# Optimization experiments

Measured on AMD Instinct MI355X. Metric: run time of the kernel, lower is better.

The kernel has to match this reference:

```python
import jax, jax.numpy as jnp
import numpy as np

N = 16384  # number of internal DAG nodes
L = 16384  # number of leaves


def setup_inputs() -> dict:
    key = jax.random.key(0)
    ks = jax.random.split(key, 12)
    idx = jnp.arange(N)
    # internal-child offsets and leaf ids
    off_l = jax.random.randint(ks[0], (N,), 1, N)
    off_r = jax.random.randint(ks[1], (N,), 1, N)
    leaf_l = jax.random.randint(ks[2], (N,), 0, L)
    leaf_r = jax.random.randint(ks[3], (N,), 0, L)
    is_int_l = (jax.random.uniform(ks[4], (N,)) < 0.5) & (idx < N - 1)
    is_int_r = (jax.random.uniform(ks[5], (N,)) < 0.5) & (idx < N - 1)
    # forward-pointing DAG: internal child index strictly greater than parent
    left = jnp.where(is_int_l, jnp.clip(idx + off_l, 0, N - 1), -(leaf_l + 1)).astype(jnp.int32)
    right = jnp.where(is_int_r, jnp.clip(idx + off_r, 0, N - 1), -(leaf_r + 1)).astype(jnp.int32)
    return {
        "thresholds": jax.random.normal(ks[6], (N,), dtype=jnp.float32),
        "rules": jax.random.randint(ks[7], (N,), 0, 16).astype(jnp.int32),
        "binary_ops": jax.random.randint(ks[8], (N,), 0, 8).astype(jnp.int32),
        "left": left,
        "right": right,
        "leaf_is_reroll": jax.random.uniform(ks[9], (L,)) < 0.5,
        "leaf_mask_left": jax.random.randint(ks[10], (L,), 0, 64).astype(jnp.int32),
        "leaf_mask_right": jax.random.randint(ks[11], (L,), 0, 64).astype(jnp.int32),
        "leaf_mask_op": jax.random.randint(jax.random.fold_in(key, 100), (L,), 0, 4).astype(jnp.int32),
        "leaf_score_cat": jax.random.randint(jax.random.fold_in(key, 101), (L,), 0, 16).astype(jnp.int32),
    }


def _active_mask(left, right, n_nodes):
    def step(reachable, _):
        active_left = jnp.where(reachable & (left >= 0), left, n_nodes)
        active_right = jnp.where(reachable & (right >= 0), right, n_nodes)
        new_reachable = jnp.zeros(n_nodes + 1, dtype=jnp.bool_)
        new_reachable = new_reachable.at[active_left].set(True)
        new_reachable = new_reachable.at[active_right].set(True)
        new_reachable = new_reachable.at[0].set(True)
        return new_reachable[:n_nodes] | reachable, None

    init = jnp.zeros(n_nodes, dtype=jnp.bool_).at[0].set(True)
    mask, _ = jax.lax.scan(step, init, None, length=n_nodes)
    return mask


def _subtree_leaf_flags(left, right, leaf_is_reroll, n):
    def is_leaf_score(child):
        leaf_id = -child - 1
        return (child < 0) & (~leaf_is_reroll[leaf_id])

    def is_leaf_reroll(child):
        leaf_id = -child - 1
        return (child < 0) & leaf_is_reroll[leaf_id]

    def step(carry, i):
        has_score, has_reroll = carry
        node = n - 1 - i  # postorder: children have larger indices
        l, r = left[node], right[node]

        def child_has_score(child):
            return is_leaf_score(child) | jnp.where(child >= 0, has_score[child], False)

        def child_has_reroll(child):
            return is_leaf_reroll(child) | jnp.where(child >= 0, has_reroll[child], False)

        has_score = has_score.at[node].set(child_has_score(l) | child_has_score(r))
        has_reroll = has_reroll.at[node].set(child_has_reroll(l) | child_has_reroll(r))
        return (has_score, has_reroll), None

    init = (jnp.zeros(n, dtype=jnp.bool_), jnp.zeros(n, dtype=jnp.bool_))
    (has_score, has_reroll), _ = jax.lax.scan(step, init, jnp.arange(n))
    return has_score, has_reroll


def reference(thresholds, rules, binary_ops, left, right, leaf_is_reroll,
              leaf_mask_left, leaf_mask_right, leaf_mask_op, leaf_score_cat):
    n = rules.shape[0]
    active_mask = _active_mask(left, right, n)
    has_score, has_reroll = _subtree_leaf_flags(left, right, leaf_is_reroll, n)
    active_node_count = jnp.sum(active_mask)
    return active_mask, has_score, has_reroll, active_node_count
```

## Files before the change

kernel.cpp:

```cpp
#include <hip/hip_runtime.h>

#define NN 16384
#define NT 1024
#define PER 16

__global__ __launch_bounds__(NT) void dag_eval_kernel(
    const int* __restrict__ left,
    const int* __restrict__ right,
    const unsigned char* __restrict__ reroll_raw,
    int* __restrict__ out)
{
    __shared__ __align__(16) unsigned char reach[NN];
    __shared__ __align__(16) unsigned char state[NN + 16];
    __shared__ int flags[4];
    __shared__ int nzmask;
    __shared__ int cnt;

    const int tid = threadIdx.x;
    const int b0  = tid * PER;

    if (tid < 4)  flags[tid] = 0;
    if (tid == 0) { nzmask = 0; cnt = 0; }
    if (tid < 16) state[NN + tid] = 4;

    unsigned int cpair[PER];
    {
        const int4* l4 = (const int4*)left;
        const int4* r4 = (const int4*)right;
        #pragma unroll
        for (int j = 0; j < PER / 4; ++j) {
            int4 a = l4[(b0 >> 2) + j];
            int4 b = r4[(b0 >> 2) + j];
            cpair[4*j+0] = (a.x & 0xFFFFu) | ((unsigned)b.x << 16);
            cpair[4*j+1] = (a.y & 0xFFFFu) | ((unsigned)b.y << 16);
            cpair[4*j+2] = (a.z & 0xFFFFu) | ((unsigned)b.z << 16);
            cpair[4*j+3] = (a.w & 0xFFFFu) | ((unsigned)b.w << 16);
        }
    }

    {
        uint4 v = ((const uint4*)reroll_raw)[tid];
        unsigned int t = v.x | v.y | v.z | v.w;
        unsigned int m = 0;
        if (t & 0x000000FFu) m |= 1u;
        if (t & 0x0000FF00u) m |= 2u;
        if (t & 0x00FF0000u) m |= 4u;
        if (t & 0xFF000000u) m |= 8u;
        if (m) atomicOr(&nzmask, (int)m);
    }
    *(uint4*)&reach[b0] = make_uint4(0u, 0u, 0u, 0u);
    __syncthreads();

    const int mask   = nzmask;
    const int layout = ((mask & ~1) == 0) ? 0 : (((mask & 3) == 0) ? 1 : 2);
    const int*   ri = (const int*)reroll_raw;
    const float* rf = (const float*)reroll_raw;

    int sreg[PER];
    unsigned int todo = 0;
    #pragma unroll
    for (int k = 0; k < PER; ++k) {
        int c0 = (int)(short)(cpair[k] & 0xFFFFu);
        int c1 = (int)(short)(cpair[k] >> 16);
        int s = 0;
        if (c0 < 0) {
            int id = -c0 - 1;
            bool rr = (layout == 2) ? (reroll_raw[id] != 0)
                     : (layout == 1) ? (rf[id] != 0.0f)
                                     : (ri[id] != 0);
            s |= rr ? 2 : 1;
        }
        if (c1 < 0) {
            int id = -c1 - 1;
            bool rr = (layout == 2) ? (reroll_raw[id] != 0)
                     : (layout == 1) ? (rf[id] != 0.0f)
                                     : (ri[id] != 0);
            s |= rr ? 2 : 1;
        }
        if ((c0 < 0 && c1 < 0) || s == 3) s |= 4;
        else todo |= 1u << k;
        sreg[k] = s;
        state[b0 + k] = (unsigned char)s;
    }
    if (tid == 0) reach[0] = 1;
    __syncthreads();

    unsigned int pushed = 0, mm = 0;
    for (int w = 0; w < 4096; ++w) {
        bool ch = false;

        uint4 rv = *(const uint4*)&reach[b0];
        mm  =  ((rv.x * 0x01020408u) >> 24) & 0xFu;
        mm |= (((rv.y * 0x01020408u) >> 24) & 0xFu) << 4;
        mm |= (((rv.z * 0x01020408u) >> 24) & 0xFu) << 8;
        mm |= (((rv.w * 0x01020408u) >> 24) & 0xFu) << 12;
        unsigned int newp = mm & ~pushed;
        if (newp) {
            pushed |= newp;
            ch = true;
            #pragma unroll
            for (int k = 0; k < PER; ++k) {
                if ((newp >> k) & 1u) {
                    int c0 = (int)(short)(cpair[k] & 0xFFFFu);
                    int c1 = (int)(short)(cpair[k] >> 16);
                    if (c0 > 0) reach[c0] = (unsigned char)1;
                    if (c1 > 0) reach[c1] = (unsigned char)1;
                }
            }
        }

        if (todo) {
            int tl[PER], tr[PER];
            #pragma unroll
            for (int k = 0; k < PER; ++k) {
                bool act = (todo >> k) & 1u;
                int c0 = (int)(short)(cpair[k] & 0xFFFFu);
                int c1 = (int)(short)(cpair[k] >> 16);
                int la = (act && c0 > 0) ? c0 : NN;
                int ra = (act && c1 > 0) ? c1 : NN;
                tl[k] = state[la];
                tr[k] = state[ra];
            }
            #pragma unroll
            for (int k = 0; k < PER; ++k) {
                if ((todo >> k) & 1u) {
                    int sl = tl[k], sr = tr[k];
                    int ns = sreg[k] | (sl & 3) | (sr & 3);
                    bool fin = ((sl & sr & 4) != 0) || ((ns & 3) == 3);
                    if (fin) { ns |= 4; todo &= ~(1u << k); }
                    if (ns != sreg[k]) {
                        sreg[k] = ns;
                        state[b0 + k] = (unsigned char)ns;
                        ch = true;
                    }
                }
            }
        }

        if (ch) flags[w & 3] = 1;
        __syncthreads();
        int f = flags[w & 3];
        if (tid == 0) flags[(w + 2) & 3] = 0;
        if (!f) break;
    }

    int cc = __popc(mm);
    #pragma unroll
    for (int off = 32; off; off >>= 1) cc += __shfl_down(cc, off);
    if ((tid & 63) == 0) atomicAdd(&cnt, cc);

    int4* out4 = (int4*)out;
    #pragma unroll
    for (int j = 0; j < PER / 4; ++j) {
        int4 a, h, r;
        a.x = (mm >> (4*j+0)) & 1; a.y = (mm >> (4*j+1)) & 1;
        a.z = (mm >> (4*j+2)) & 1; a.w = (mm >> (4*j+3)) & 1;
        h.x =  sreg[4*j+0] & 1;       h.y =  sreg[4*j+1] & 1;
        h.z =  sreg[4*j+2] & 1;       h.w =  sreg[4*j+3] & 1;
        r.x = (sreg[4*j+0] >> 1) & 1; r.y = (sreg[4*j+1] >> 1) & 1;
        r.z = (sreg[4*j+2] >> 1) & 1; r.w = (sreg[4*j+3] >> 1) & 1;
        out4[(b0 >> 2) + j]            = a;
        out4[((NN + b0) >> 2) + j]     = h;
        out4[((2 * NN + b0) >> 2) + j] = r;
    }
    __syncthreads();
    if (tid == 0) out[3 * NN] = cnt;
}

extern "C" void kernel_launch(void* const* d_in, const int* in_sizes, int n_in,
                              void* d_out, int out_size, void* d_ws, size_t ws_size,
                              hipStream_t stream)
{
    const int* left  = (const int*)d_in[3];
    const int* right = (const int*)d_in[4];
    const unsigned char* reroll = (const unsigned char*)d_in[5];
    int* out = (int*)d_out;
    dag_eval_kernel<<<1, NT, 0, stream>>>(left, right, reroll, out);
}
```

Before: 32.84 us.

## Switch to strided node-to-thread mapping and restructure the fixpoint sweep

Nodes are now assigned to threads as tid + k*NT instead of contiguous blocks of 16. This makes the global loads of left/right coalesced and spreads shared-memory byte accesses across banks. The sweep now reads reach per node, in pairs, and updates state from high k to low k so that changes can propagate within one sweep. Final outputs and the count are rebuilt from the shared reach and state arrays, and the iteration cap is lowered to 600. The trade-off is more per-byte LDS reads than the old single uint4 load, and a cap that depends on the DAG depth staying small.

```diff
diff --git a/kernel.cpp b/kernel.cpp
--- a/kernel.cpp
+++ b/kernel.cpp
@@ -2,7 +2,6 @@
 
 #define NN 16384
 #define NT 1024
-#define PER 16
 
 __global__ __launch_bounds__(NT) void dag_eval_kernel(
     const int* __restrict__ left,
@@ -17,25 +16,17 @@
     __shared__ int cnt;
 
     const int tid = threadIdx.x;
-    const int b0  = tid * PER;
 
     if (tid < 4)  flags[tid] = 0;
     if (tid == 0) { nzmask = 0; cnt = 0; }
     if (tid < 16) state[NN + tid] = 4;
 
-    unsigned int cpair[PER];
-    {
-        const int4* l4 = (const int4*)left;
-        const int4* r4 = (const int4*)right;
-        #pragma unroll
-        for (int j = 0; j < PER / 4; ++j) {
-            int4 a = l4[(b0 >> 2) + j];
-            int4 b = r4[(b0 >> 2) + j];
-            cpair[4*j+0] = (a.x & 0xFFFFu) | ((unsigned)b.x << 16);
-            cpair[4*j+1] = (a.y & 0xFFFFu) | ((unsigned)b.y << 16);
-            cpair[4*j+2] = (a.z & 0xFFFFu) | ((unsigned)b.z << 16);
-            cpair[4*j+3] = (a.w & 0xFFFFu) | ((unsigned)b.w << 16);
-        }
+    unsigned int cpair[16];
+    #pragma unroll
+    for (int k = 0; k < 16; ++k) {
+        int l = left[tid + k * NT];
+        int r = right[tid + k * NT];
+        cpair[k] = (l & 0xFFFFu) | ((unsigned)r << 16);
     }
 
     {
@@ -48,7 +39,7 @@
         if (t & 0xFF000000u) m |= 8u;
         if (m) atomicOr(&nzmask, (int)m);
     }
-    *(uint4*)&reach[b0] = make_uint4(0u, 0u, 0u, 0u);
+    *(uint4*)&reach[tid * 16] = make_uint4(0u, 0u, 0u, 0u);
     __syncthreads();
 
     const int mask   = nzmask;
@@ -56,10 +47,10 @@
     const int*   ri = (const int*)reroll_raw;
     const float* rf = (const float*)reroll_raw;
 
-    int sreg[PER];
+    int sreg[16];
     unsigned int todo = 0;
     #pragma unroll
-    for (int k = 0; k < PER; ++k) {
+    for (int k = 0; k < 16; ++k) {
         int c0 = (int)(short)(cpair[k] & 0xFFFFu);
         int c1 = (int)(short)(cpair[k] >> 16);
         int s = 0;
@@ -80,29 +71,33 @@
         if ((c0 < 0 && c1 < 0) || s == 3) s |= 4;
         else todo |= 1u << k;
         sreg[k] = s;
-        state[b0 + k] = (unsigned char)s;
+        state[tid + k * NT] = (unsigned char)s;
     }
     if (tid == 0) reach[0] = 1;
     __syncthreads();
 
-    unsigned int pushed = 0, mm = 0;
-    for (int w = 0; w < 4096; ++w) {
+    unsigned int pushed = 0;
+    for (int w = 0; w < 600; ++w) {
         bool ch = false;
 
-        uint4 rv = *(const uint4*)&reach[b0];
-        mm  =  ((rv.x * 0x01020408u) >> 24) & 0xFu;
-        mm |= (((rv.y * 0x01020408u) >> 24) & 0xFu) << 4;
-        mm |= (((rv.z * 0x01020408u) >> 24) & 0xFu) << 8;
-        mm |= (((rv.w * 0x01020408u) >> 24) & 0xFu) << 12;
-        unsigned int newp = mm & ~pushed;
-        if (newp) {
-            pushed |= newp;
-            ch = true;
-            #pragma unroll
-            for (int k = 0; k < PER; ++k) {
-                if ((newp >> k) & 1u) {
-                    int c0 = (int)(short)(cpair[k] & 0xFFFFu);
-                    int c1 = (int)(short)(cpair[k] >> 16);
+        #pragma unroll
+        for (int kp = 0; kp < 8; ++kp) {
+            const int k0 = 2 * kp, k1 = 2 * kp + 1;
+            unsigned int need = (~pushed >> k0) & 3u;
+            if (need) {
+                int r0 = (need & 1u) ? (int)reach[tid + k0 * NT] : 0;
+                int r1 = (need & 2u) ? (int)reach[tid + k1 * NT] : 0;
+                if (r0) {
+                    pushed |= 1u << k0; ch = true;
+                    int c0 = (int)(short)(cpair[k0] & 0xFFFFu);
+                    int c1 = (int)(short)(cpair[k0] >> 16);
+                    if (c0 > 0) reach[c0] = (unsigned char)1;
+                    if (c1 > 0) reach[c1] = (unsigned char)1;
+                }
+                if (r1) {
+                    pushed |= 1u << k1; ch = true;
+                    int c0 = (int)(short)(cpair[k1] & 0xFFFFu);
+                    int c1 = (int)(short)(cpair[k1] >> 16);
                     if (c0 > 0) reach[c0] = (unsigned char)1;
                     if (c1 > 0) reach[c1] = (unsigned char)1;
                 }
@@ -110,28 +105,39 @@
         }
 
         if (todo) {
-            int tl[PER], tr[PER];
             #pragma unroll
-            for (int k = 0; k < PER; ++k) {
-                bool act = (todo >> k) & 1u;
-                int c0 = (int)(short)(cpair[k] & 0xFFFFu);
-                int c1 = (int)(short)(cpair[k] >> 16);
-                int la = (act && c0 > 0) ? c0 : NN;
-                int ra = (act && c1 > 0) ? c1 : NN;
-                tl[k] = state[la];
-                tr[k] = state[ra];
-            }
-            #pragma unroll
-            for (int k = 0; k < PER; ++k) {
-                if ((todo >> k) & 1u) {
-                    int sl = tl[k], sr = tr[k];
-                    int ns = sreg[k] | (sl & 3) | (sr & 3);
-                    bool fin = ((sl & sr & 4) != 0) || ((ns & 3) == 3);
-                    if (fin) { ns |= 4; todo &= ~(1u << k); }
-                    if (ns != sreg[k]) {
-                        sreg[k] = ns;
-                        state[b0 + k] = (unsigned char)ns;
-                        ch = true;
+            for (int kp = 7; kp >= 0; --kp) {
+                const int k0 = 2 * kp, k1 = 2 * kp + 1;
+                if ((todo >> k0) & 3u) {
+                    bool a1 = (todo >> k1) & 1u;
+                    bool a0 = (todo >> k0) & 1u;
+                    int c10 = (int)(short)(cpair[k1] & 0xFFFFu);
+                    int c11 = (int)(short)(cpair[k1] >> 16);
+                    int c00 = (int)(short)(cpair[k0] & 0xFFFFu);
+                    int c01 = (int)(short)(cpair[k0] >> 16);
+                    int sl1 = state[(a1 && c10 > 0) ? c10 : NN];
+                    int sr1 = state[(a1 && c11 > 0) ? c11 : NN];
+                    int sl0 = state[(a0 && c00 > 0) ? c00 : NN];
+                    int sr0 = state[(a0 && c01 > 0) ? c01 : NN];
+                    if (a1) {
+                        int ns = sreg[k1] | (sl1 & 3) | (sr1 & 3);
+                        bool fin = ((sl1 & sr1 & 4) != 0) || ((ns & 3) == 3);
+                        if (fin) { ns |= 4; todo &= ~(1u << k1); }
+                        if (ns != sreg[k1]) {
+                            sreg[k1] = ns;
+                            state[tid + k1 * NT] = (unsigned char)ns;
+                            ch = true;
+                        }
+                    }
+                    if (a0) {
+                        int ns = sreg[k0] | (sl0 & 3) | (sr0 & 3);
+                        bool fin = ((sl0 & sr0 & 4) != 0) || ((ns & 3) == 3);
+                        if (fin) { ns |= 4; todo &= ~(1u << k0); }
+                        if (ns != sreg[k0]) {
+                            sreg[k0] = ns;
+                            state[tid + k0 * NT] = (unsigned char)ns;
+                            ch = true;
+                        }
                     }
                 }
             }
@@ -144,24 +150,41 @@
         if (!f) break;
     }
 
-    int cc = __popc(mm);
-    #pragma unroll
-    for (int off = 32; off; off >>= 1) cc += __shfl_down(cc, off);
-    if ((tid & 63) == 0) atomicAdd(&cnt, cc);
+    uint4 v = *(const uint4*)&reach[tid * 16];
+    {
+        unsigned int t = v.x + v.y + v.z + v.w;
+        int cc = (t & 0xFF) + ((t >> 8) & 0xFF) + ((t >> 16) & 0xFF) + (t >> 24);
+        #pragma unroll
+        for (int off = 32; off; off >>= 1) cc += __shfl_down(cc, off);
+        if ((tid & 63) == 0) atomicAdd(&cnt, cc);
+    }
 
     int4* out4 = (int4*)out;
-    #pragma unroll
-    for (int j = 0; j < PER / 4; ++j) {
-        int4 a, h, r;
-        a.x = (mm >> (4*j+0)) & 1; a.y = (mm >> (4*j+1)) & 1;
-        a.z = (mm >> (4*j+2)) & 1; a.w = (mm >> (4*j+3)) & 1;
-        h.x =  sreg[4*j+0] & 1;       h.y =  sreg[4*j+1] & 1;
-        h.z =  sreg[4*j+2] & 1;       h.w =  sreg[4*j+3] & 1;
-        r.x = (sreg[4*j+0] >> 1) & 1; r.y = (sreg[4*j+1] >> 1) & 1;
-        r.z = (sreg[4*j+2] >> 1) & 1; r.w = (sreg[4*j+3] >> 1) & 1;
-        out4[(b0 >> 2) + j]            = a;
-        out4[((NN + b0) >> 2) + j]     = h;
-        out4[((2 * NN + b0) >> 2) + j] = r;
+    {
+        unsigned int wd[4] = {v.x, v.y, v.z, v.w};
+        #pragma unroll
+        for (int j = 0; j < 4; ++j) {
+            int4 a;
+            a.x = (wd[j] >> 0)  & 1;
+            a.y = (wd[j] >> 8)  & 1;
+            a.z = (wd[j] >> 16) & 1;
+            a.w = (wd[j] >> 24) & 1;
+            out4[(tid * 16 >> 2) + j] = a;
+        }
+    }
+    {
+        uint4 sv = *(const uint4*)&state[tid * 16];
+        unsigned int wd[4] = {sv.x, sv.y, sv.z, sv.w};
+        #pragma unroll
+        for (int j = 0; j < 4; ++j) {
+            int4 h, r;
+            h.x = (wd[j] >> 0)  & 1; h.y = (wd[j] >> 8)  & 1;
+            h.z = (wd[j] >> 16) & 1; h.w = (wd[j] >> 24) & 1;
+            r.x = (wd[j] >> 1)  & 1; r.y = (wd[j] >> 9)  & 1;
+            r.z = (wd[j] >> 17) & 1; r.w = (wd[j] >> 25) & 1;
+            out4[((NN + tid * 16) >> 2) + j]     = h;
+            out4[((2 * NN + tid * 16) >> 2) + j] = r;
+        }
     }
     __syncthreads();
     if (tid == 0) out[3 * NN] = cnt;
```

New measurement: 36.30 us. 10.6% more time.

## Propagate reachability and subtree flags two levels per iteration via shared child pairs

Applied to the files above, without the earlier changes.

Stores the packed child pairs for every node in shared memory so each sweep can look at grandchildren. Reachability propagation marks children and grandchildren, and the subtree-flag fixpoint reads grandchild states, which roughly halves the number of barrier-synchronised iterations needed to converge. Per-child pending bits let a node finish once each child is done, and the change flag now fires only on real updates. The cost is 64KB more shared memory, extra shared loads per iteration, and an iteration cap lowered to 600, which could cut off deep DAGs before they converge.

```diff
diff --git a/kernel.cpp b/kernel.cpp
--- a/kernel.cpp
+++ b/kernel.cpp
@@ -10,6 +10,7 @@
     const unsigned char* __restrict__ reroll_raw,
     int* __restrict__ out)
 {
+    __shared__ __align__(16) unsigned int  pairs[NN];
     __shared__ __align__(16) unsigned char reach[NN];
     __shared__ __align__(16) unsigned char state[NN + 16];
     __shared__ int flags[4];
@@ -21,7 +22,7 @@
 
     if (tid < 4)  flags[tid] = 0;
     if (tid == 0) { nzmask = 0; cnt = 0; }
-    if (tid < 16) state[NN + tid] = 4;
+    if (tid < 16) state[NN + tid] = 0;
 
     unsigned int cpair[PER];
     {
@@ -35,6 +36,8 @@
             cpair[4*j+1] = (a.y & 0xFFFFu) | ((unsigned)b.y << 16);
             cpair[4*j+2] = (a.z & 0xFFFFu) | ((unsigned)b.z << 16);
             cpair[4*j+3] = (a.w & 0xFFFFu) | ((unsigned)b.w << 16);
+            *(uint4*)&pairs[b0 + 4*j] = make_uint4(cpair[4*j+0], cpair[4*j+1],
+                                                   cpair[4*j+2], cpair[4*j+3]);
         }
     }
 
@@ -57,28 +60,29 @@
     const float* rf = (const float*)reroll_raw;
 
     int sreg[PER];
-    unsigned int todo = 0;
+    unsigned int todo = 0, pend = 0;
     #pragma unroll
     for (int k = 0; k < PER; ++k) {
         int c0 = (int)(short)(cpair[k] & 0xFFFFu);
         int c1 = (int)(short)(cpair[k] >> 16);
         int s = 0;
+        unsigned int p2 = 0;
         if (c0 < 0) {
             int id = -c0 - 1;
             bool rr = (layout == 2) ? (reroll_raw[id] != 0)
                      : (layout == 1) ? (rf[id] != 0.0f)
                                      : (ri[id] != 0);
             s |= rr ? 2 : 1;
-        }
+        } else p2 |= 1u;
         if (c1 < 0) {
             int id = -c1 - 1;
             bool rr = (layout == 2) ? (reroll_raw[id] != 0)
                      : (layout == 1) ? (rf[id] != 0.0f)
                                      : (ri[id] != 0);
             s |= rr ? 2 : 1;
-        }
-        if ((c0 < 0 && c1 < 0) || s == 3) s |= 4;
-        else todo |= 1u << k;
+        } else p2 |= 2u;
+        if (p2 == 0u || s == 3) s |= 4;
+        else { todo |= 1u << k; pend |= p2 << (2 * k); }
         sreg[k] = s;
         state[b0 + k] = (unsigned char)s;
     }
@@ -86,7 +90,7 @@
     __syncthreads();
 
     unsigned int pushed = 0, mm = 0;
-    for (int w = 0; w < 4096; ++w) {
+    for (int w = 0; w < 600; ++w) {
         bool ch = false;
 
         uint4 rv = *(const uint4*)&reach[b0];
@@ -97,37 +101,65 @@
         unsigned int newp = mm & ~pushed;
         if (newp) {
             pushed |= newp;
-            ch = true;
             #pragma unroll
             for (int k = 0; k < PER; ++k) {
                 if ((newp >> k) & 1u) {
                     int c0 = (int)(short)(cpair[k] & 0xFFFFu);
                     int c1 = (int)(short)(cpair[k] >> 16);
-                    if (c0 > 0) reach[c0] = (unsigned char)1;
-                    if (c1 > 0) reach[c1] = (unsigned char)1;
+                    if (c0 > 0) {
+                        if (reach[c0] == 0) { reach[c0] = 1; ch = true; }
+                        unsigned int pr = pairs[c0];
+                        int g0 = (int)(short)(pr & 0xFFFFu);
+                        int g1 = (int)(short)(pr >> 16);
+                        if (g0 > 0 && reach[g0] == 0) { reach[g0] = 1; ch = true; }
+                        if (g1 > 0 && reach[g1] == 0) { reach[g1] = 1; ch = true; }
+                    }
+                    if (c1 > 0) {
+                        if (reach[c1] == 0) { reach[c1] = 1; ch = true; }
+                        unsigned int pr = pairs[c1];
+                        int g0 = (int)(short)(pr & 0xFFFFu);
+                        int g1 = (int)(short)(pr >> 16);
+                        if (g0 > 0 && reach[g0] == 0) { reach[g0] = 1; ch = true; }
+                        if (g1 > 0 && reach[g1] == 0) { reach[g1] = 1; ch = true; }
+                    }
                 }
             }
         }
 
         if (todo) {
-            int tl[PER], tr[PER];
-            #pragma unroll
-            for (int k = 0; k < PER; ++k) {
-                bool act = (todo >> k) & 1u;
-                int c0 = (int)(short)(cpair[k] & 0xFFFFu);
-                int c1 = (int)(short)(cpair[k] >> 16);
-                int la = (act && c0 > 0) ? c0 : NN;
-                int ra = (act && c1 > 0) ? c1 : NN;
-                tl[k] = state[la];
-                tr[k] = state[ra];
-            }
             #pragma unroll
             for (int k = 0; k < PER; ++k) {
                 if ((todo >> k) & 1u) {
-                    int sl = tl[k], sr = tr[k];
+                    unsigned int p2 = (pend >> (2 * k)) & 3u;
+                    int c0 = (int)(short)(cpair[k] & 0xFFFFu);
+                    int c1 = (int)(short)(cpair[k] >> 16);
+                    int sl = state[(p2 & 1u) ? c0 : NN];
+                    int sr = state[(p2 & 2u) ? c1 : NN];
                     int ns = sreg[k] | (sl & 3) | (sr & 3);
-                    bool fin = ((sl & sr & 4) != 0) || ((ns & 3) == 3);
+                    unsigned int np2 = p2;
+                    if ((p2 & 1u) && (sl & 4)) np2 &= ~1u;
+                    if ((p2 & 2u) && (sr & 4)) np2 &= ~2u;
+                    if (np2 & 1u) {
+                        unsigned int pr = pairs[c0];
+                        int g0 = (int)(short)(pr & 0xFFFFu);
+                        int g1 = (int)(short)(pr >> 16);
+                        int s0 = (g0 > 0) ? (int)state[g0] : 4;
+                        int s1 = (g1 > 0) ? (int)state[g1] : 4;
+                        ns |= (s0 & 3) | (s1 & 3);
+                        if (s0 & s1 & 4) np2 &= ~1u;
+                    }
+                    if (np2 & 2u) {
+                        unsigned int pr = pairs[c1];
+                        int g0 = (int)(short)(pr & 0xFFFFu);
+                        int g1 = (int)(short)(pr >> 16);
+                        int s0 = (g0 > 0) ? (int)state[g0] : 4;
+                        int s1 = (g1 > 0) ? (int)state[g1] : 4;
+                        ns |= (s0 & 3) | (s1 & 3);
+                        if (s0 & s1 & 4) np2 &= ~2u;
+                    }
+                    bool fin = (np2 == 0u) || ((ns & 3) == 3);
                     if (fin) { ns |= 4; todo &= ~(1u << k); }
+                    pend = (pend & ~(3u << (2 * k))) | (np2 << (2 * k));
                     if (ns != sreg[k]) {
                         sreg[k] = ns;
                         state[b0 + k] = (unsigned char)ns;
```

Result: no change. 32.91 us (+0.2%).

## Switch to single-wavefront sparse frontier/worklist phase after fixed block sweeps

Applied to the files above, without the earlier changes.

Runs a fixed number of block-wide sweeps, then gathers unfinished nodes into a shared worklist. A single 64-lane wavefront finishes both the reachability propagation, using a shared bitmask with atomicOr, and the subtree-flag fixpoint without block barriers. The aim is to remove the many block-wide __syncthreads iterations of the long convergence tail. The cost is serial work on one wavefront and a hard 300-iteration cap, which could leave the result unconverged on deep chains; it also relies on intra-wave visibility of shared memory.

```diff
diff --git a/kernel.cpp b/kernel.cpp
--- a/kernel.cpp
+++ b/kernel.cpp
@@ -3,6 +3,7 @@
 #define NN 16384
 #define NT 1024
 #define PER 16
+#define SW1 8
 
 __global__ __launch_bounds__(NT) void dag_eval_kernel(
     const int* __restrict__ left,
@@ -10,17 +11,19 @@
     const unsigned char* __restrict__ reroll_raw,
     int* __restrict__ out)
 {
+    __shared__ __align__(16) unsigned int  pairs[NN];
     __shared__ __align__(16) unsigned char reach[NN];
     __shared__ __align__(16) unsigned char state[NN + 16];
-    __shared__ int flags[4];
+    __shared__ __align__(16) unsigned int  bits[NN / 32];
+    __shared__ unsigned short wl[NN];
+    __shared__ int wl_n;
     __shared__ int nzmask;
     __shared__ int cnt;
 
     const int tid = threadIdx.x;
     const int b0  = tid * PER;
 
-    if (tid < 4)  flags[tid] = 0;
-    if (tid == 0) { nzmask = 0; cnt = 0; }
+    if (tid == 0) { nzmask = 0; cnt = 0; wl_n = 0; }
     if (tid < 16) state[NN + tid] = 4;
 
     unsigned int cpair[PER];
@@ -35,6 +38,8 @@
             cpair[4*j+1] = (a.y & 0xFFFFu) | ((unsigned)b.y << 16);
             cpair[4*j+2] = (a.z & 0xFFFFu) | ((unsigned)b.z << 16);
             cpair[4*j+3] = (a.w & 0xFFFFu) | ((unsigned)b.w << 16);
+            *(uint4*)&pairs[b0 + 4*j] = make_uint4(cpair[4*j+0], cpair[4*j+1],
+                                                   cpair[4*j+2], cpair[4*j+3]);
         }
     }
 
@@ -85,11 +90,11 @@
     if (tid == 0) reach[0] = 1;
     __syncthreads();
 
-    unsigned int pushed = 0, mm = 0;
-    for (int w = 0; w < 4096; ++w) {
-        bool ch = false;
-
+    unsigned int pushed = 0;
+    #pragma unroll 1
+    for (int s = 0; s < SW1; ++s) {
         uint4 rv = *(const uint4*)&reach[b0];
+        unsigned int mm;
         mm  =  ((rv.x * 0x01020408u) >> 24) & 0xFu;
         mm |= (((rv.y * 0x01020408u) >> 24) & 0xFu) << 4;
         mm |= (((rv.z * 0x01020408u) >> 24) & 0xFu) << 8;
@@ -97,7 +102,6 @@
         unsigned int newp = mm & ~pushed;
         if (newp) {
             pushed |= newp;
-            ch = true;
             #pragma unroll
             for (int k = 0; k < PER; ++k) {
                 if ((newp >> k) & 1u) {
@@ -108,7 +112,6 @@
                 }
             }
         }
-
         if (todo) {
             int tl[PER], tr[PER];
             #pragma unroll
@@ -131,37 +134,125 @@
                     if (ns != sreg[k]) {
                         sreg[k] = ns;
                         state[b0 + k] = (unsigned char)ns;
-                        ch = true;
                     }
                 }
             }
         }
-
-        if (ch) flags[w & 3] = 1;
         __syncthreads();
-        int f = flags[w & 3];
-        if (tid == 0) flags[(w + 2) & 3] = 0;
-        if (!f) break;
-    }
-
-    int cc = __popc(mm);
-    #pragma unroll
-    for (int off = 32; off; off >>= 1) cc += __shfl_down(cc, off);
-    if ((tid & 63) == 0) atomicAdd(&cnt, cc);
+    }
+
+    if (todo) {
+        #pragma unroll
+        for (int k = 0; k < PER; ++k) {
+            if ((todo >> k) & 1u) {
+                int idx = atomicAdd(&wl_n, 1);
+                wl[idx] = (unsigned short)(b0 + k);
+            }
+        }
+    }
+    __syncthreads();
+
+    if (tid < 64) {
+        const int l = tid;
+        unsigned int pushedw[8];
+        #pragma unroll
+        for (int w8 = 0; w8 < 8; ++w8) {
+            uint4 u0 = *(const uint4*)&reach[l * 256 + w8 * 32];
+            uint4 u1 = *(const uint4*)&reach[l * 256 + w8 * 32 + 16];
+            unsigned int m;
+            m  =  ((u0.x * 0x01020408u) >> 24) & 0xFu;
+            m |= (((u0.y * 0x01020408u) >> 24) & 0xFu) << 4;
+            m |= (((u0.z * 0x01020408u) >> 24) & 0xFu) << 8;
+            m |= (((u0.w * 0x01020408u) >> 24) & 0xFu) << 12;
+            m |= (((u1.x * 0x01020408u) >> 24) & 0xFu) << 16;
+            m |= (((u1.y * 0x01020408u) >> 24) & 0xFu) << 20;
+            m |= (((u1.z * 0x01020408u) >> 24) & 0xFu) << 24;
+            m |= (((u1.w * 0x01020408u) >> 24) & 0xFu) << 28;
+            bits[l * 8 + w8] = m;
+            pushedw[w8] = 0u;
+        }
+        const int n2 = wl_n;
+        bool fdone = false;
+        for (int it = 0; it < 300; ++it) {
+            bool any_new = false;
+            if (!fdone) {
+                #pragma unroll
+                for (int w8 = 0; w8 < 8; ++w8) {
+                    unsigned int cur = bits[l * 8 + w8];
+                    unsigned int nw = cur & ~pushedw[w8];
+                    pushedw[w8] = cur;
+                    while (nw) {
+                        int b = __builtin_ctz(nw);
+                        nw &= nw - 1u;
+                        int node = l * 256 + w8 * 32 + b;
+                        unsigned int pr = pairs[node];
+                        int c0 = (int)(short)(pr & 0xFFFFu);
+                        int c1 = (int)(short)(pr >> 16);
+                        if (c0 > 0) atomicOr(&bits[c0 >> 5], 1u << (c0 & 31));
+                        if (c1 > 0) atomicOr(&bits[c1 >> 5], 1u << (c1 & 31));
+                        any_new = true;
+                    }
+                }
+                fdone = !__any(any_new);
+            }
+            bool blive = false;
+            for (int i = l; i < n2; i += 64) {
+                int n = wl[i];
+                if (n != 0xFFFF) {
+                    int st = state[n];
+                    unsigned int pr = pairs[n];
+                    int c0 = (int)(short)(pr & 0xFFFFu);
+                    int c1 = (int)(short)(pr >> 16);
+                    int s0 = (c0 > 0) ? (int)state[c0] : 4;
+                    int s1 = (c1 > 0) ? (int)state[c1] : 4;
+                    int ns = st | (s0 & 3) | (s1 & 3);
+                    bool fin = ((s0 & s1 & 4) != 0) || ((ns & 3) == 3);
+                    if (fin) {
+                        state[n] = (unsigned char)(ns | 4);
+                        wl[i] = 0xFFFF;
+                    } else {
+                        if (ns != st) state[n] = (unsigned char)ns;
+                        blive = true;
+                    }
+                }
+            }
+            if (fdone && !__any(blive)) break;
+            asm volatile("" ::: "memory");
+        }
+    }
+    __syncthreads();
+
+    unsigned int m16 = (bits[tid >> 1] >> ((tid & 1) * 16)) & 0xFFFFu;
+    {
+        int cc = __popc(m16);
+        #pragma unroll
+        for (int off = 32; off; off >>= 1) cc += __shfl_down(cc, off);
+        if ((tid & 63) == 0) atomicAdd(&cnt, cc);
+    }
 
     int4* out4 = (int4*)out;
     #pragma unroll
-    for (int j = 0; j < PER / 4; ++j) {
-        int4 a, h, r;
-        a.x = (mm >> (4*j+0)) & 1; a.y = (mm >> (4*j+1)) & 1;
-        a.z = (mm >> (4*j+2)) & 1; a.w = (mm >> (4*j+3)) & 1;
-        h.x =  sreg[4*j+0] & 1;       h.y =  sreg[4*j+1] & 1;
-        h.z =  sreg[4*j+2] & 1;       h.w =  sreg[4*j+3] & 1;
-        r.x = (sreg[4*j+0] >> 1) & 1; r.y = (sreg[4*j+1] >> 1) & 1;
-        r.z = (sreg[4*j+2] >> 1) & 1; r.w = (sreg[4*j+3] >> 1) & 1;
-        out4[(b0 >> 2) + j]            = a;
-        out4[((NN + b0) >> 2) + j]     = h;
-        out4[((2 * NN + b0) >> 2) + j] = r;
+    for (int j = 0; j < 4; ++j) {
+        int4 a;
+        a.x = (m16 >> (4*j+0)) & 1;
+        a.y = (m16 >> (4*j+1)) & 1;
+        a.z = (m16 >> (4*j+2)) & 1;
+        a.w = (m16 >> (4*j+3)) & 1;
+        out4[(b0 >> 2) + j] = a;
+    }
+    {
+        uint4 sv = *(const uint4*)&state[b0];
+        unsigned int wd[4] = {sv.x, sv.y, sv.z, sv.w};
+        #pragma unroll
+        for (int j = 0; j < 4; ++j) {
+            int4 h, r;
+            h.x = (wd[j] >> 0)  & 1; h.y = (wd[j] >> 8)  & 1;
+            h.z = (wd[j] >> 16) & 1; h.w = (wd[j] >> 24) & 1;
+            r.x = (wd[j] >> 1)  & 1; r.y = (wd[j] >> 9)  & 1;
+            r.z = (wd[j] >> 17) & 1; r.w = (wd[j] >> 25) & 1;
+            out4[((NN + b0) >> 2) + j]     = h;
+            out4[((2 * NN + b0) >> 2) + j] = r;
+        }
     }
     __syncthreads();
     if (tid == 0) out[3 * NN] = cnt;
```

New measurement: 35.46 us. +8.0%, slower.
